# Performance work log

Measured on AMD Instinct MI355X. Metric: run time of the kernel, lower is better.

The kernel has to match this reference:

```python
import jax, jax.numpy as jnp
import numpy as np

N_LAYERS = 4
D_MODEL = 1024
D_INNER = 2048
DT_RANK = 64
D_STATE = 16
D_CONV = 4
EPS = 1e-5


def _rms(x, w):
    return x * jax.lax.rsqrt(jnp.mean(x * x, axis=-1, keepdims=True) + EPS) * w


def _silu(x):
    return x * jax.nn.sigmoid(x)


def setup_inputs() -> dict:
    key = jax.random.key(0)
    ks = jax.random.split(key, 8)
    B, L = 2, 1024
    s = 0.02
    nl, dm, di = N_LAYERS, D_MODEL, D_INNER
    return {
        "x": jax.random.normal(ks[0], (B, L, dm), dtype=jnp.float32),
        "norm_w": jnp.ones((nl, dm), dtype=jnp.float32),
        "W_in": jax.random.normal(ks[1], (nl, 2 * di, dm), dtype=jnp.float32) * s,
        "conv_w": jax.random.normal(ks[2], (nl, di, D_CONV), dtype=jnp.float32) * s,
        "conv_b": jnp.zeros((nl, di), dtype=jnp.float32),
        "W_x": jax.random.normal(ks[3], (nl, DT_RANK + 2 * D_STATE, di), dtype=jnp.float32) * s,
        "W_dt": jax.random.normal(ks[4], (nl, di, DT_RANK), dtype=jnp.float32) * (DT_RANK ** -0.5),
        "b_dt": jax.random.normal(ks[5], (nl, di), dtype=jnp.float32) - 3.0,  # softplus -> small dt, like inv-softplus init
        "A_log": jax.random.uniform(ks[6], (nl, di, D_STATE), dtype=jnp.float32) * 2.0,  # A = -exp(A_log) in [-7.4, -1]
        "D": jnp.ones((nl, di), dtype=jnp.float32),
        "W_out": jax.random.normal(ks[7], (nl, dm, di), dtype=jnp.float32) * s,
    }


def reference(x, norm_w, W_in, conv_w, conv_b, W_x, W_dt, b_dt, A_log, D, W_out):
    nl = W_in.shape[0]
    L = x.shape[1]
    dc = conv_w.shape[-1]
    n = A_log.shape[-1]
    rk = W_dt.shape[-1]

    def combine(left, right):
        a1, b1 = left
        a2, b2 = right
        return a2 * a1, a2 * b1 + b2

    for i in range(nl):
        h = _rms(x, norm_w[i])
        xz = jnp.einsum('bld,ed->ble', h, W_in[i])          # [B,L,2*Di]
        xi, z = jnp.split(xz, 2, axis=-1)
        # causal depthwise conv1d (padding=dc-1, keep first L outputs)
        xp = jnp.pad(xi, ((0, 0), (dc - 1, 0), (0, 0)))
        xc = conv_b[i] + sum(xp[:, k:k + L, :] * conv_w[i][:, k] for k in range(dc))
        xc = _silu(xc)
        # SSM parameterization
        dbc = jnp.einsum('bld,ed->ble', xc, W_x[i])          # [B,L,rk+2n]
        delta, Bm, Cm = jnp.split(dbc, [rk, rk + n], axis=-1)
        delta = jax.nn.softplus(jnp.einsum('blr,dr->bld', delta, W_dt[i]) + b_dt[i])  # [B,L,Di]
        A = -jnp.exp(A_log[i])                               # [Di,N]
        deltaA = jnp.exp(delta[..., None] * A)               # [B,L,Di,N]
        BX = (delta * xc)[..., None] * Bm[:, :, None, :]     # [B,L,Di,N]
        # parallel scan: h_t = deltaA_t * h_{t-1} + BX_t
        _, hs = jax.lax.associative_scan(combine, (deltaA, BX), axis=1)
        y = jnp.einsum('bldn,bln->bld', hs, Cm) + D[i] * xc
        out = jnp.einsum('bld,ed->ble', y * _silu(z), W_out[i])
        x = x + out
    return x
```

## Files before the change

kernel.cpp:

```cpp
#include <hip/hip_runtime.h>
#include <hip/hip_bf16.h>
#include <math.h>

#define NL 4
#define DM 1024
#define DI 2048
#define RK 64
#define NS 16
#define LSEQ 1024
#define BATCH 2
#define MROWS (BATCH*LSEQ)
#define NCHUNK 32
#define LC 32

typedef __attribute__((ext_vector_type(8))) short bf16x8;
typedef __attribute__((ext_vector_type(4))) float f32x4;

__device__ __forceinline__ float bf2f(unsigned short u){
  union { unsigned int i; float f; } v; v.i = ((unsigned int)u) << 16; return v.f;
}
__device__ __forceinline__ unsigned short f2bf(float f){
  union { float f; unsigned int i; } v; v.f = f;
  unsigned int r = v.i + 0x7fffu + ((v.i >> 16) & 1u);
  return (unsigned short)(r >> 16);
}
__device__ __forceinline__ float sigmoidf_(float x){ return 1.0f / (1.0f + __expf(-x)); }
__device__ __forceinline__ float softplusf_(float x){ return (x > 20.0f) ? x : log1pf(__expf(x)); }

__device__ __forceinline__ void gl2lds16(const void* g, void* l) {
  __builtin_amdgcn_global_load_lds((__attribute__((address_space(1))) void*)g,
                                   (__attribute__((address_space(3))) void*)l,
                                   16, 0, 0);
}

template<int BM, int BN, int WAVES_M, int WAVES_N, int EPI>
__global__ __launch_bounds__(256)
void gemm_bt(const unsigned short* __restrict__ A, const unsigned short* __restrict__ W,
             void* __restrict__ C, const float* __restrict__ bias,
             int M, int N, int K, int ldc, int kslices)
{
  constexpr int MT = BM / (WAVES_M * 16);
  constexpr int NT = BN / (WAVES_N * 16);
  __shared__ __align__(16) unsigned short As[BM * 64];
  __shared__ __align__(16) unsigned short Bs[BN * 64];

  const int tid  = threadIdx.x;
  const int wave = tid >> 6;
  const int lane = tid & 63;
  const int wm   = wave / WAVES_N;
  const int wn   = wave % WAVES_N;
  const int quad = lane >> 4;
  const int l16  = lane & 15;
  const int srow = lane >> 3;
  const int scol = ((lane & 7) ^ srow) * 8;

  const int m0 = blockIdx.x * BM;
  const int n0 = blockIdx.y * BN;
  const int Ks = K / kslices;
  const int kb = blockIdx.z * Ks;

  f32x4 acc[MT][NT];
  #pragma unroll
  for (int i = 0; i < MT; i++)
    #pragma unroll
    for (int j = 0; j < NT; j++)
      acc[i][j] = (f32x4){0.f, 0.f, 0.f, 0.f};

  for (int k0 = kb; k0 < kb + Ks; k0 += 64) {
    const unsigned short* Ab = A + (size_t)m0 * K + k0;
    #pragma unroll
    for (int i = 0; i < BM / 32; i++) {
      int c = i * 4 + wave;
      gl2lds16(Ab + (size_t)(c * 8 + srow) * K + scol, As + c * 512);
    }
    const unsigned short* Wb = W + (size_t)n0 * K + k0;
    #pragma unroll
    for (int i = 0; i < BN / 32; i++) {
      int c = i * 4 + wave;
      gl2lds16(Wb + (size_t)(c * 8 + srow) * K + scol, Bs + c * 512);
    }
    __syncthreads();

    #pragma unroll
    for (int h = 0; h < 2; h++) {
      bf16x8 af[MT], bfr[NT];
      #pragma unroll
      for (int mt = 0; mt < MT; mt++) {
        int rA = wm * MT * 16 + mt * 16 + l16;
        af[mt] = *(const bf16x8*)(As + rA * 64 + (((h * 4 + quad) ^ (rA & 7)) << 3));
      }
      #pragma unroll
      for (int nt = 0; nt < NT; nt++) {
        int rB = wn * NT * 16 + nt * 16 + l16;
        bfr[nt] = *(const bf16x8*)(Bs + rB * 64 + (((h * 4 + quad) ^ (rB & 7)) << 3));
      }
      #pragma unroll
      for (int mt = 0; mt < MT; mt++)
        #pragma unroll
        for (int nt = 0; nt < NT; nt++)
          acc[mt][nt] = __builtin_amdgcn_mfma_f32_16x16x32_bf16(af[mt], bfr[nt], acc[mt][nt], 0, 0, 0);
    }
    __syncthreads();
  }

  const size_t slice_off = (size_t)blockIdx.z * M * ldc;
  #pragma unroll
  for (int mt = 0; mt < MT; mt++) {
    #pragma unroll
    for (int nt = 0; nt < NT; nt++) {
      int n = n0 + wn * NT * 16 + nt * 16 + l16;
      #pragma unroll
      for (int r = 0; r < 4; r++) {
        int m = m0 + wm * MT * 16 + mt * 16 + quad * 4 + r;
        float v = acc[mt][nt][r];
        size_t off = (size_t)m * ldc + n;
        if constexpr (EPI == 0)      ((unsigned short*)C)[off] = f2bf(v);
        else if constexpr (EPI == 2) ((float*)C)[off] = softplusf_(v + bias[n]);
        else                         ((float*)C)[slice_off + off] = v;
      }
    }
  }
}

__global__ __launch_bounds__(256)
void reduce4_kernel(const float* __restrict__ part, float* __restrict__ x)
{
  const size_t MN = (size_t)MROWS * DM;
  int i = blockIdx.x * 256 + threadIdx.x;
  float4 a = ((const float4*)part)[i];
  float4 b = ((const float4*)(part + MN))[i];
  float4 c = ((const float4*)(part + 2 * MN))[i];
  float4 d = ((const float4*)(part + 3 * MN))[i];
  float4 o = ((float4*)x)[i];
  o.x += a.x + b.x + c.x + d.x;
  o.y += a.y + b.y + c.y + d.y;
  o.z += a.z + b.z + c.z + d.z;
  o.w += a.w + b.w + c.w + d.w;
  ((float4*)x)[i] = o;
}

__global__ __launch_bounds__(256)
void reduce2_kernel(const float* __restrict__ part, float* __restrict__ dbc,
                    unsigned short* __restrict__ dt_bf)
{
  const int MN = MROWS * 96;
  int i = blockIdx.x * 256 + threadIdx.x;
  float v = part[i] + part[MN + i] + part[2 * MN + i] + part[3 * MN + i];
  dbc[i] = v;
  int m = i / 96, c = i - m * 96;
  if (c < RK) dt_bf[m * RK + c] = f2bf(v);
}

__global__ __launch_bounds__(256)
void rmsnorm_kernel(const float* __restrict__ x, const float* __restrict__ w,
                    unsigned short* __restrict__ h)
{
  const int row = blockIdx.x;
  const float4 a = ((const float4*)(x + (size_t)row * DM))[threadIdx.x];
  float ss = a.x*a.x + a.y*a.y + a.z*a.z + a.w*a.w;
  #pragma unroll
  for (int o = 32; o > 0; o >>= 1) ss += __shfl_down(ss, o);
  __shared__ float red[4];
  if ((threadIdx.x & 63) == 0) red[threadIdx.x >> 6] = ss;
  __syncthreads();
  float rs = rsqrtf((red[0] + red[1] + red[2] + red[3]) * (1.0f / DM) + 1e-5f);
  const float4 wv = ((const float4*)w)[threadIdx.x];
  ushort4 o4;
  o4.x = f2bf(a.x * rs * wv.x);
  o4.y = f2bf(a.y * rs * wv.y);
  o4.z = f2bf(a.z * rs * wv.z);
  o4.w = f2bf(a.w * rs * wv.w);
  ((ushort4*)(h + (size_t)row * DM))[threadIdx.x] = o4;
}

__global__ __launch_bounds__(256)
void conv_silu_kernel(const unsigned short* __restrict__ xz,
                      const float* __restrict__ cw, const float* __restrict__ cb,
                      unsigned short* __restrict__ xc)
{
  int idx = blockIdx.x * 256 + threadIdx.x;
  int d = idx & (DI - 1);
  int t = (idx >> 11) & (LSEQ - 1);
  int b = idx >> 21;
  const float4 w4 = ((const float4*)cw)[d];
  const float wk[4] = {w4.x, w4.y, w4.z, w4.w};
  const unsigned short* xi = xz + (size_t)b * LSEQ * (2 * DI) + d;
  float acc = cb[d];
  #pragma unroll
  for (int k = 0; k < 4; k++) {
    int tt = t - 3 + k;
    if (tt >= 0) acc += bf2f(xi[(size_t)tt * (2 * DI)]) * wk[k];
  }
  xc[idx] = f2bf(acc * sigmoidf_(acc));
}

__global__ void convert_all_kernel(const float* __restrict__ W_in, unsigned short* __restrict__ Win_bf,
                                   const float* __restrict__ W_x,  unsigned short* __restrict__ Wx_bf,
                                   const float* __restrict__ W_dt, unsigned short* __restrict__ Wdt_bf,
                                   const float* __restrict__ W_out,unsigned short* __restrict__ Wout_bf)
{
  const float* src[4]  = {W_in, W_x, W_dt, W_out};
  unsigned short* dst[4] = {Win_bf, Wx_bf, Wdt_bf, Wout_bf};
  const int n4[4] = {NL*2*DI*DM/4, NL*96*DI/4, NL*DI*RK/4, NL*DM*DI/4};
  for (int s = 0; s < 4; s++) {
    int stride = gridDim.x * 256;
    for (int i = blockIdx.x * 256 + threadIdx.x; i < n4[s]; i += stride) {
      float4 v = ((const float4*)src[s])[i];
      ushort4 o; o.x = f2bf(v.x); o.y = f2bf(v.y); o.z = f2bf(v.z); o.w = f2bf(v.w);
      ((ushort4*)dst[s])[i] = o;
    }
  }
}

__global__ __launch_bounds__(256)
void scan1_kernel(const float* __restrict__ delta, const unsigned short* __restrict__ xc,
                  const float* __restrict__ dbc, const float* __restrict__ A_log,
                  float* __restrict__ hend, float* __restrict__ sumd)
{
  const int d = blockIdx.x * 256 + threadIdx.x;
  const int c = blockIdx.y;
  const int b = blockIdx.z;
  const int t0 = c * LC;
  __shared__ float bc[LC][32];
  #pragma unroll
  for (int i = 0; i < (LC * 32) / 256; i++) {
    int f = i * 256 + threadIdx.x;
    int r = f >> 5, col = f & 31;
    bc[r][col] = dbc[(size_t)(b * LSEQ + t0 + r) * 96 + 64 + col];
  }
  float Av[NS], h[NS];
  #pragma unroll
  for (int n = 0; n < NS; n++) { Av[n] = -__expf(A_log[(size_t)d * NS + n]); h[n] = 0.f; }
  __syncthreads();
  float sd = 0.f;
  for (int t = 0; t < LC; t++) {
    size_t ix = (size_t)(b * LSEQ + t0 + t) * DI + d;
    float dt = delta[ix];
    float xcv = bf2f(xc[ix]);
    sd += dt;
    float dx = dt * xcv;
    #pragma unroll
    for (int n = 0; n < NS; n++) {
      float da = __expf(dt * Av[n]);
      h[n] = da * h[n] + dx * bc[t][n];
    }
  }
  size_t base = ((size_t)(b * NCHUNK + c) * NS) * DI + d;
  #pragma unroll
  for (int n = 0; n < NS; n++) hend[base + (size_t)n * DI] = h[n];
  sumd[(size_t)(b * NCHUNK + c) * DI + d] = sd;
}

__global__ __launch_bounds__(256)
void scan2_kernel(const float* __restrict__ A_log, const float* __restrict__ hend,
                  const float* __restrict__ sumd, float* __restrict__ hin)
{
  int g = blockIdx.x * 256 + threadIdx.x;
  int b = g >> 11;
  int d = g & (DI - 1);
  float Av[NS], H[NS];
  #pragma unroll
  for (int n = 0; n < NS; n++) { Av[n] = -__expf(A_log[(size_t)d * NS + n]); H[n] = 0.f; }
  for (int c = 0; c < NCHUNK; c++) {
    size_t base = ((size_t)(b * NCHUNK + c) * NS) * DI + d;
    float sd = sumd[(size_t)(b * NCHUNK + c) * DI + d];
    #pragma unroll
    for (int n = 0; n < NS; n++) {
      hin[base + (size_t)n * DI] = H[n];
      float da = __expf(Av[n] * sd);
      H[n] = da * H[n] + hend[base + (size_t)n * DI];
    }
  }
}

__global__ __launch_bounds__(256)
void scan3_kernel(const float* __restrict__ delta, const unsigned short* __restrict__ xc,
                  const float* __restrict__ dbc, const float* __restrict__ A_log,
                  const float* __restrict__ hin, const float* __restrict__ Dvec,
                  const unsigned short* __restrict__ xz, unsigned short* __restrict__ g)
{
  const int d = blockIdx.x * 256 + threadIdx.x;
  const int c = blockIdx.y;
  const int b = blockIdx.z;
  const int t0 = c * LC;
  __shared__ float bc[LC][32];
  #pragma unroll
  for (int i = 0; i < (LC * 32) / 256; i++) {
    int f = i * 256 + threadIdx.x;
    int r = f >> 5, col = f & 31;
    bc[r][col] = dbc[(size_t)(b * LSEQ + t0 + r) * 96 + 64 + col];
  }
  float Av[NS], h[NS];
  size_t base = ((size_t)(b * NCHUNK + c) * NS) * DI + d;
  #pragma unroll
  for (int n = 0; n < NS; n++) {
    Av[n] = -__expf(A_log[(size_t)d * NS + n]);
    h[n] = hin[base + (size_t)n * DI];
  }
  const float Dd = Dvec[d];
  __syncthreads();
  for (int t = 0; t < LC; t++) {
    size_t ix = (size_t)(b * LSEQ + t0 + t) * DI + d;
    float dt = delta[ix];
    float xcv = bf2f(xc[ix]);
    float dx = dt * xcv;
    float y = Dd * xcv;
    #pragma unroll
    for (int n = 0; n < NS; n++) {
      float da = __expf(dt * Av[n]);
      h[n] = da * h[n] + dx * bc[t][n];
      y += h[n] * bc[t][16 + n];
    }
    float zv = bf2f(xz[(size_t)(b * LSEQ + t0 + t) * (2 * DI) + DI + d]);
    g[ix] = f2bf(y * (zv * sigmoidf_(zv)));
  }
}

extern "C" void kernel_launch(void* const* d_in, const int* in_sizes, int n_in,
                              void* d_out, int out_size, void* d_ws, size_t ws_size,
                              hipStream_t stream)
{
  const float* x_in   = (const float*)d_in[0];
  const float* norm_w = (const float*)d_in[1];
  const float* W_in   = (const float*)d_in[2];
  const float* conv_w = (const float*)d_in[3];
  const float* conv_b = (const float*)d_in[4];
  const float* W_x    = (const float*)d_in[5];
  const float* W_dt   = (const float*)d_in[6];
  const float* b_dt   = (const float*)d_in[7];
  const float* A_log  = (const float*)d_in[8];
  const float* Dv     = (const float*)d_in[9];
  const float* W_out  = (const float*)d_in[10];
  float* x = (float*)d_out;

  char* p = (char*)d_ws;
  auto alloc = [&](size_t bytes) {
    void* r = (void*)p;
    p += (bytes + 255) & ~(size_t)255;
    return r;
  };
  unsigned short* Win_bf  = (unsigned short*)alloc((size_t)NL * 2 * DI * DM * 2);
  unsigned short* Wx_bf   = (unsigned short*)alloc((size_t)NL * 96 * DI * 2);
  unsigned short* Wdt_bf  = (unsigned short*)alloc((size_t)NL * DI * RK * 2);
  unsigned short* Wout_bf = (unsigned short*)alloc((size_t)NL * DM * DI * 2);
  unsigned short* h_bf    = (unsigned short*)alloc((size_t)MROWS * DM * 2);
  unsigned short* xz_bf   = (unsigned short*)alloc((size_t)MROWS * 2 * DI * 2);
  unsigned short* xc_bf   = (unsigned short*)alloc((size_t)MROWS * DI * 2);
  float*          dbc     = (float*)alloc((size_t)MROWS * 96 * 4);
  unsigned short* dt_bf   = (unsigned short*)alloc((size_t)MROWS * RK * 2);
  unsigned short* g_bf    = (unsigned short*)alloc((size_t)MROWS * DI * 2);
  float*          delta   = (float*)alloc((size_t)MROWS * DI * 4);
  float*          hend    = (float*)alloc((size_t)BATCH * NCHUNK * NS * DI * 4);
  float*          hin     = (float*)alloc((size_t)BATCH * NCHUNK * NS * DI * 4);
  float*          sumd    = (float*)alloc((size_t)BATCH * NCHUNK * DI * 4);
  float* part2 = delta;
  float* part4 = delta;

  hipMemcpyAsync(x, x_in, (size_t)MROWS * DM * 4, hipMemcpyDeviceToDevice, stream);

  convert_all_kernel<<<2048, 256, 0, stream>>>(W_in, Win_bf, W_x, Wx_bf,
                                               W_dt, Wdt_bf, W_out, Wout_bf);

  for (int l = 0; l < NL; l++) {
    const unsigned short* Win_l  = Win_bf  + (size_t)l * 2 * DI * DM;
    const unsigned short* Wx_l   = Wx_bf   + (size_t)l * 96 * DI;
    const unsigned short* Wdt_l  = Wdt_bf  + (size_t)l * DI * RK;
    const unsigned short* Wout_l = Wout_bf + (size_t)l * DM * DI;

    rmsnorm_kernel<<<MROWS, 256, 0, stream>>>(x, norm_w + (size_t)l * DM, h_bf);

    gemm_bt<128, 128, 2, 2, 0><<<dim3(MROWS / 128, (2 * DI) / 128), 256, 0, stream>>>(
        h_bf, Win_l, xz_bf, nullptr, MROWS, 2 * DI, DM, 2 * DI, 1);

    conv_silu_kernel<<<(BATCH * LSEQ * DI) / 256, 256, 0, stream>>>(
        xz_bf, conv_w + (size_t)l * DI * 4, conv_b + (size_t)l * DI, xc_bf);

    gemm_bt<64, 96, 4, 1, 4><<<dim3(MROWS / 64, 1, 4), 256, 0, stream>>>(
        xc_bf, Wx_l, part2, nullptr, MROWS, 96, DI, 96, 4);
    reduce2_kernel<<<(MROWS * 96) / 256, 256, 0, stream>>>(part2, dbc, dt_bf);

    gemm_bt<128, 128, 2, 2, 2><<<dim3(MROWS / 128, DI / 128), 256, 0, stream>>>(
        dt_bf, Wdt_l, delta, b_dt + (size_t)l * DI, MROWS, DI, RK, DI, 1);

    scan1_kernel<<<dim3(DI / 256, NCHUNK, BATCH), 256, 0, stream>>>(
        delta, xc_bf, dbc, A_log + (size_t)l * DI * NS, hend, sumd);
    scan2_kernel<<<(BATCH * DI) / 256, 256, 0, stream>>>(
        A_log + (size_t)l * DI * NS, hend, sumd, hin);
    scan3_kernel<<<dim3(DI / 256, NCHUNK, BATCH), 256, 0, stream>>>(
        delta, xc_bf, dbc, A_log + (size_t)l * DI * NS, hin, Dv + (size_t)l * DI, xz_bf, g_bf);

    gemm_bt<128, 128, 2, 2, 4><<<dim3(MROWS / 128, DM / 128, 4), 256, 0, stream>>>(
        g_bf, Wout_l, part4, nullptr, MROWS, DM, DI, DM, 4);
    reduce4_kernel<<<(MROWS * DM) / 1024, 256, 0, stream>>>(part4, x);
  }
}
```

Baseline: 959.0 us.

## Replace dt-projection MFMA GEMM with fused FP32 kernel reading dbc directly

Removes the bf16 dt staging buffer and instead computes the delta projection plus bias and softplus in a dedicated small-K kernel that reads the fp32 dbc rows directly. Each block stages 8 rows of dt and a transposed 256-column weight tile in LDS and accumulates with scalar FMAs. This drops one write/read of the dt buffer and the generic GEMM epilogue path, at the cost of giving up MFMA and reloading the weight tile for every 8-row block.

New measurement: 851.5 us. 1.13x faster.

```diff
diff --git a/kernel.cpp b/kernel.cpp
--- a/kernel.cpp
+++ b/kernel.cpp
@@ -115,11 +115,67 @@
         float v = acc[mt][nt][r];
         size_t off = (size_t)m * ldc + n;
         if constexpr (EPI == 0)      ((unsigned short*)C)[off] = f2bf(v);
-        else if constexpr (EPI == 2) ((float*)C)[off] = softplusf_(v + bias[n]);
         else                         ((float*)C)[slice_off + off] = v;
       }
     }
   }
+}
+
+#define G3R 8
+#define G3C 256
+#define G3P 264
+__global__ __launch_bounds__(256)
+void gemm3_fused(const float* __restrict__ dbc, const unsigned short* __restrict__ Wdt,
+                 const float* __restrict__ b_dt, float* __restrict__ delta)
+{
+  __shared__ float dts[G3R][RK];
+  __shared__ __align__(16) unsigned short Ws[RK][G3P];
+  const int tid = threadIdx.x;
+  const int m0 = blockIdx.x * G3R;
+  const int c0 = blockIdx.y * G3C;
+
+  {
+    int r = tid >> 5, k = (tid & 31) * 2;
+    float2 v = *(const float2*)(dbc + (size_t)(m0 + r) * 96 + k);
+    dts[r][k] = v.x; dts[r][k + 1] = v.y;
+  }
+  {
+    const unsigned short* wrow = Wdt + (size_t)(c0 + tid) * RK;
+    #pragma unroll
+    for (int ch = 0; ch < 8; ch++) {
+      union { bf16x8 v; unsigned short u[8]; } w;
+      w.v = *(const bf16x8*)(wrow + ch * 8);
+      #pragma unroll
+      for (int j = 0; j < 8; j++) Ws[ch * 8 + j][tid] = w.u[j];
+    }
+  }
+  __syncthreads();
+
+  const int r  = tid >> 5;
+  const int cg = tid & 31;
+  float acc[8] = {0.f, 0.f, 0.f, 0.f, 0.f, 0.f, 0.f, 0.f};
+  #pragma unroll 4
+  for (int k = 0; k < RK; k++) {
+    float a = dts[r][k];
+    union { bf16x8 v; unsigned short u[8]; } w;
+    w.v = *(const bf16x8*)&Ws[k][cg * 8];
+    #pragma unroll
+    for (int j = 0; j < 8; j++) acc[j] += a * bf2f(w.u[j]);
+  }
+
+  const int m = m0 + r, c = c0 + cg * 8;
+  float4 b0 = *(const float4*)(b_dt + c);
+  float4 b1 = *(const float4*)(b_dt + c + 4);
+  float bb[8] = {b0.x, b0.y, b0.z, b0.w, b1.x, b1.y, b1.z, b1.w};
+  float out[8];
+  #pragma unroll
+  for (int j = 0; j < 8; j++) {
+    float v = acc[j] + bb[j];
+    out[j] = (v > 15.0f) ? v : __logf(1.0f + __expf(v));
+  }
+  float* dp = delta + (size_t)m * DI + c;
+  *(float4*)dp       = (float4){out[0], out[1], out[2], out[3]};
+  *(float4*)(dp + 4) = (float4){out[4], out[5], out[6], out[7]};
 }
 
 __global__ __launch_bounds__(256)
@@ -140,15 +196,11 @@
 }
 
 __global__ __launch_bounds__(256)
-void reduce2_kernel(const float* __restrict__ part, float* __restrict__ dbc,
-                    unsigned short* __restrict__ dt_bf)
+void reduce2_kernel(const float* __restrict__ part, float* __restrict__ dbc)
 {
   const int MN = MROWS * 96;
   int i = blockIdx.x * 256 + threadIdx.x;
-  float v = part[i] + part[MN + i] + part[2 * MN + i] + part[3 * MN + i];
-  dbc[i] = v;
-  int m = i / 96, c = i - m * 96;
-  if (c < RK) dt_bf[m * RK + c] = f2bf(v);
+  dbc[i] = part[i] + part[MN + i] + part[2 * MN + i] + part[3 * MN + i];
 }
 
 __global__ __launch_bounds__(256)
@@ -347,7 +399,6 @@
   unsigned short* xz_bf   = (unsigned short*)alloc((size_t)MROWS * 2 * DI * 2);
   unsigned short* xc_bf   = (unsigned short*)alloc((size_t)MROWS * DI * 2);
   float*          dbc     = (float*)alloc((size_t)MROWS * 96 * 4);
-  unsigned short* dt_bf   = (unsigned short*)alloc((size_t)MROWS * RK * 2);
   unsigned short* g_bf    = (unsigned short*)alloc((size_t)MROWS * DI * 2);
   float*          delta   = (float*)alloc((size_t)MROWS * DI * 4);
   float*          hend    = (float*)alloc((size_t)BATCH * NCHUNK * NS * DI * 4);
@@ -377,10 +428,10 @@
 
     gemm_bt<64, 96, 4, 1, 4><<<dim3(MROWS / 64, 1, 4), 256, 0, stream>>>(
         xc_bf, Wx_l, part2, nullptr, MROWS, 96, DI, 96, 4);
-    reduce2_kernel<<<(MROWS * 96) / 256, 256, 0, stream>>>(part2, dbc, dt_bf);
-
-    gemm_bt<128, 128, 2, 2, 2><<<dim3(MROWS / 128, DI / 128), 256, 0, stream>>>(
-        dt_bf, Wdt_l, delta, b_dt + (size_t)l * DI, MROWS, DI, RK, DI, 1);
+    reduce2_kernel<<<(MROWS * 96) / 256, 256, 0, stream>>>(part2, dbc);
+
+    gemm3_fused<<<dim3(MROWS / G3R, DI / G3C), 256, 0, stream>>>(
+        dbc, Wdt_l, b_dt + (size_t)l * DI, delta);
 
     scan1_kernel<<<dim3(DI / 256, NCHUNK, BATCH), 256, 0, stream>>>(
         delta, xc_bf, dbc, A_log + (size_t)l * DI * NS, hend, sumd);
```
